# Kernel tuning notes

Measured on AMD Instinct MI355X. Metric: run time of the kernel, lower is better.

Reference implementation:

```python
import jax, jax.numpy as jnp
import numpy as np

# Module hyperparams (from init_kwargs)
MAX_DISP = 4
DILA = 1
P = 2 * MAX_DISP // DILA + 1  # patch_size = 9 -> 81 output channels


def setup_inputs() -> dict:
    key = jax.random.key(0)
    k0, k1 = jax.random.split(key)
    B, C, H, W = 4, 256, 96, 160
    return {
        "fmap0": jax.random.normal(k0, (B, C, H, W), dtype=jnp.float32),
        "fmap1": jax.random.normal(k1, (B, C, H, W), dtype=jnp.float32),
    }


def reference(fmap0, fmap1):
    """SpatialCorrelationSampler(kernel_size=1, patch_size=P, stride=1,
    padding=0, dilation=1, dilation_patch=DILA), reshaped to (B, P*P, H, W).

    corr[b, p, y, x] = sum_c fmap0[b,c,y,x] * fmap1[b,c,y+dy_p,x+dx_p]
    with (dy,dx) in {-MAX_DISP..MAX_DISP step DILA}; out-of-bounds -> 0
    (no channel normalization, matching the CUDA sampler).
    """
    B, C, H, W = fmap0.shape
    D = MAX_DISP
    # Zero-pad fmap1 so every displacement is a static-size slice.
    padded = jnp.pad(fmap1, ((0, 0), (0, 0), (D, D), (D, D)))
    oy, ox = jnp.meshgrid(jnp.arange(P) * DILA, jnp.arange(P) * DILA, indexing="ij")
    offs = jnp.stack([oy.ravel(), ox.ravel()], axis=1)  # (P*P, 2)

    def one_disp(off):
        # window of fmap1 shifted by (off - D): (B, C, H, W)
        win = jax.lax.dynamic_slice(padded, (0, 0, off[0], off[1]), (B, C, H, W))
        return jnp.einsum("bchw,bchw->bhw", fmap0, win)

    corr = jax.lax.map(one_disp, offs)  # (P*P, B, H, W), avoids P^2*C blowup
    return jnp.transpose(corr, (1, 0, 2, 3))  # (B, P*P, H, W)
```

## Files before the change

### kernel.cpp

```cpp
#include <hip/hip_runtime.h>


#define Bn 4
#define Cn 256
#define Hn 96
#define Wn 160
#define HWn (Hn * Wn)
#define NP 81
#define TY 16
#define TX 16
#define CCH 8
#define NSTAGE (Cn / CCH)
#define WROWS (TY + 8)
#define SEGS 6
#define LROW 28
#define F1C (WROWS * LROW)
#define BUF (CCH * F1C)
#define NT 576
#define F1STG (CCH * HWn / 4)

__global__ __launch_bounds__(NT, 2) void corr_kernel(const float* __restrict__ f0,
                                                     const float* __restrict__ f1,
                                                     float* __restrict__ out) {
    __shared__ __align__(16) float lds[2 * BUF];

    const int tid  = threadIdx.x;
    const int wave = tid >> 6;
    const int lane = tid & 63;
    const int r    = lane >> 2;
    const int g    = lane & 3;

    const int blk = blockIdx.x;
    const int xcd = blk & 7;
    const int it  = blk >> 3;
    const int b   = xcd >> 1;
    const int ty  = (xcd & 1) * 3 + it / 10;
    const int tx  = it % 10;
    const int y0  = ty * TY;
    const int x0  = tx * TX;

    const int scc  = tid / (WROWS * SEGS);
    const int srm  = tid - scc * (WROWS * SEGS);
    const int srr  = srm / SEGS;
    const int sseg = srm - srr * SEGS;
    const int sgy  = y0 - 4 + srr;
    const int sgx  = x0 - 4 + sseg * 4;
    const bool sval = (sgy >= 0) && (sgy < Hn) && (sgx >= 0) && (sgx < Wn);
    const int slidx = (scc * F1C + srr * LROW + sseg * 4) >> 2;
    const int sgidx = sval ? ((((b * Cn + scc) * Hn + sgy) * Wn + sgx) >> 2) : 0;

    const float4* __restrict__ f1v = (const float4*)f1;
    float4* lv = (float4*)lds;

    float4 p1a = make_float4(0.f, 0.f, 0.f, 0.f), p1b = p1a;
    if (sval) { p1a = f1v[sgidx]; p1b = f1v[sgidx + HWn]; }

    const float* f0s = f0 + ((b * Cn) * Hn + y0 + r) * Wn + x0 + g * 4;
    float4 p0[CCH];
#pragma unroll
    for (int cc = 0; cc < CCH; ++cc) p0[cc] = *(const float4*)(f0s + cc * HWn);

    float acc[9][4];
#pragma unroll
    for (int i = 0; i < 9; ++i)
#pragma unroll
        for (int j = 0; j < 4; ++j) acc[i][j] = 0.f;

    for (int s = 0; s < NSTAGE; ++s) {
        float4* buf = lv + (s & 1) * (BUF / 4);
        buf[slidx]       = p1a;
        buf[slidx + F1C] = p1b;
        __syncthreads();

        const int ns = (s + 1 < NSTAGE) ? s + 1 : NSTAGE - 1;
        float4 n1a = make_float4(0.f, 0.f, 0.f, 0.f), n1b = n1a;
        if (sval) { n1a = f1v[sgidx + ns * F1STG]; n1b = f1v[sgidx + ns * F1STG + HWn]; }
        float4 n0[CCH];
#pragma unroll
        for (int cc = 0; cc < CCH; ++cc)
            n0[cc] = *(const float4*)(f0s + (ns * CCH + cc) * HWn);

        const float* base = &lds[(s & 1) * BUF + (r + wave) * LROW + g * 4];
#pragma unroll
        for (int cc = 0; cc < CCH; ++cc) {
            const float* wr = base + cc * F1C;
            float4 w0 = *(const float4*)(wr);
            float4 w1 = *(const float4*)(wr + 4);
            float4 w2 = *(const float4*)(wr + 8);
            float av[4]  = {p0[cc].x, p0[cc].y, p0[cc].z, p0[cc].w};
            float wv[12] = {w0.x, w0.y, w0.z, w0.w, w1.x, w1.y, w1.z, w1.w,
                            w2.x, w2.y, w2.z, w2.w};
#pragma unroll
            for (int dx = 0; dx < 9; ++dx)
#pragma unroll
                for (int rx = 0; rx < 4; ++rx)
                    acc[dx][rx] = fmaf(av[rx], wv[rx + dx], acc[dx][rx]);
        }

        p1a = n1a; p1b = n1b;
#pragma unroll
        for (int cc = 0; cc < CCH; ++cc) p0[cc] = n0[cc];
    }

    const int orow = ((b * NP + wave * 9) * Hn + y0 + r) * Wn + x0 + g * 4;
#pragma unroll
    for (int dx = 0; dx < 9; ++dx)
        *(float4*)(out + orow + dx * HWn) =
            make_float4(acc[dx][0], acc[dx][1], acc[dx][2], acc[dx][3]);
}

extern "C" void kernel_launch(void* const* d_in, const int* in_sizes, int n_in,
                              void* d_out, int out_size, void* d_ws, size_t ws_size,
                              hipStream_t stream) {
    const float* f0 = (const float*)d_in[0];
    const float* f1 = (const float*)d_in[1];
    float* out = (float*)d_out;
    corr_kernel<<<dim3(240), NT, 0, stream>>>(f0, f1, out);
}
```

Baseline: 182.8 us.

## Rewrite correlation as fp16 MFMA banded matmul over channel chunks

Replaces the scalar FP32 FMA correlation kernel with one that converts both feature maps to fp16 and computes 16x32 banded products with 16x16x32 f16 MFMA instructions. Each wave handles one output row, and a 32-wide window is kept per displacement row, so only the diagonal band of each product is written out. Tiling, grid size (480 blocks of 512 threads) and the LDS layout all change. Much of the computed tile is thrown away, and the fp16 inputs reduce accuracy of a 256-channel sum.

```diff
diff --git a/kernel.cpp b/kernel.cpp
--- a/kernel.cpp
+++ b/kernel.cpp
@@ -1,5 +1,9 @@
 #include <hip/hip_runtime.h>
 
+
+using pkh2_t  = __attribute__((ext_vector_type(2))) __fp16;
+using half8_t = __attribute__((ext_vector_type(8))) _Float16;
+using f32x4_t = __attribute__((ext_vector_type(4))) float;
 
 #define Bn 4
 #define Cn 256
@@ -7,106 +11,120 @@
 #define Wn 160
 #define HWn (Hn * Wn)
 #define NP 81
-#define TY 16
-#define TX 16
-#define CCH 8
-#define NSTAGE (Cn / CCH)
-#define WROWS (TY + 8)
-#define SEGS 6
-#define LROW 28
-#define F1C (WROWS * LROW)
-#define BUF (CCH * F1C)
-#define NT 576
-#define F1STG (CCH * HWn / 4)
+#define YS 8
+#define MT 16
+#define KC 32
+#define NCHK (Cn / KC)
+#define WR (YS + 8)
+#define WP 32
+#define PXD 20
+#define ROWD (WP * PXD)
+#define BUFD (WR * ROWD)
+#define NT 512
 
-__global__ __launch_bounds__(NT, 2) void corr_kernel(const float* __restrict__ f0,
-                                                     const float* __restrict__ f1,
-                                                     float* __restrict__ out) {
-    __shared__ __align__(16) float lds[2 * BUF];
+__global__ __launch_bounds__(NT, 2) void corr_mfma(const float* __restrict__ f0,
+                                                   const float* __restrict__ f1,
+                                                   float* __restrict__ out) {
+    __shared__ __align__(16) unsigned int lds[BUFD];
 
     const int tid  = threadIdx.x;
-    const int wave = tid >> 6;
+    const int w    = tid >> 6;
     const int lane = tid & 63;
-    const int r    = lane >> 2;
-    const int g    = lane & 3;
+    const int q    = lane >> 4;
+    const int n    = lane & 15;
 
     const int blk = blockIdx.x;
     const int xcd = blk & 7;
     const int it  = blk >> 3;
     const int b   = xcd >> 1;
-    const int ty  = (xcd & 1) * 3 + it / 10;
-    const int tx  = it % 10;
-    const int y0  = ty * TY;
-    const int x0  = tx * TX;
+    const int ys  = (xcd & 1) * 6 + it / 10;
+    const int xt  = it % 10;
+    const int y0  = ys * YS;
+    const int x0  = xt * MT;
+    const int y   = y0 + w;
 
-    const int scc  = tid / (WROWS * SEGS);
-    const int srm  = tid - scc * (WROWS * SEGS);
-    const int srr  = srm / SEGS;
-    const int sseg = srm - srr * SEGS;
-    const int sgy  = y0 - 4 + srr;
-    const int sgx  = x0 - 4 + sseg * 4;
-    const bool sval = (sgy >= 0) && (sgy < Hn) && (sgx >= 0) && (sgx < Wn);
-    const int slidx = (scc * F1C + srr * LROW + sseg * 4) >> 2;
-    const int sgidx = sval ? ((((b * Cn + scc) * Hn + sgy) * Wn + sgx) >> 2) : 0;
+    const int rr  = tid >> 5;
+    const int pxg = (tid >> 2) & 7;
+    const int cs  = tid & 3;
+    const int gy  = y0 - 4 + rr;
+    const int gx  = x0 - 8 + pxg * 4;
+    const bool sv = (gy >= 0) && (gy < Hn) && (gx >= 0) && (gx < Wn);
+    const float4* __restrict__ f1v = (const float4*)f1;
+    const int sg0 = sv ? ((((b * Cn) * Hn + gy) * Wn + gx) >> 2) : 0;
+    const int ldw = rr * ROWD + (pxg * 4) * PXD + cs * 4;
 
-    const float4* __restrict__ f1v = (const float4*)f1;
-    float4* lv = (float4*)lds;
+    const float* __restrict__ f0p = f0 + (b * Cn) * HWn + y * Wn + x0 + n;
 
-    float4 p1a = make_float4(0.f, 0.f, 0.f, 0.f), p1b = p1a;
-    if (sval) { p1a = f1v[sgidx]; p1b = f1v[sgidx + HWn]; }
+    f32x4_t acc[9][2];
+#pragma unroll
+    for (int d = 0; d < 9; ++d)
+#pragma unroll
+        for (int t = 0; t < 2; ++t) acc[d][t] = (f32x4_t){0.f, 0.f, 0.f, 0.f};
 
-    const float* f0s = f0 + ((b * Cn) * Hn + y0 + r) * Wn + x0 + g * 4;
-    float4 p0[CCH];
+    float4 F[8];
+    float  A[8];
 #pragma unroll
-    for (int cc = 0; cc < CCH; ++cc) p0[cc] = *(const float4*)(f0s + cc * HWn);
+    for (int j = 0; j < 8; ++j) {
+        const int c = cs * 8 + j;
+        F[j] = sv ? f1v[sg0 + c * (HWn / 4)] : make_float4(0.f, 0.f, 0.f, 0.f);
+        A[j] = f0p[(q * 8 + j) * HWn];
+    }
 
-    float acc[9][4];
+    for (int ch = 0; ch < NCHK; ++ch) {
+        __syncthreads();
 #pragma unroll
-    for (int i = 0; i < 9; ++i)
+        for (int i = 0; i < 4; ++i) {
+            union { pkh2_t h2[4]; uint4 u4; } u;
 #pragma unroll
-        for (int j = 0; j < 4; ++j) acc[i][j] = 0.f;
-
-    for (int s = 0; s < NSTAGE; ++s) {
-        float4* buf = lv + (s & 1) * (BUF / 4);
-        buf[slidx]       = p1a;
-        buf[slidx + F1C] = p1b;
+            for (int k = 0; k < 4; ++k) {
+                const float lo = ((const float*)&F[2 * k])[i];
+                const float hi = ((const float*)&F[2 * k + 1])[i];
+                u.h2[k] = __builtin_amdgcn_cvt_pkrtz(lo, hi);
+            }
+            *(uint4*)&lds[ldw + i * PXD] = u.u4;
+        }
+        union { pkh2_t h2[4]; half8_t h8; } ua;
+#pragma unroll
+        for (int k = 0; k < 4; ++k)
+            ua.h2[k] = __builtin_amdgcn_cvt_pkrtz(A[2 * k], A[2 * k + 1]);
+        const half8_t afrag = ua.h8;
         __syncthreads();
 
-        const int ns = (s + 1 < NSTAGE) ? s + 1 : NSTAGE - 1;
-        float4 n1a = make_float4(0.f, 0.f, 0.f, 0.f), n1b = n1a;
-        if (sval) { n1a = f1v[sgidx + ns * F1STG]; n1b = f1v[sgidx + ns * F1STG + HWn]; }
-        float4 n0[CCH];
+        if (ch + 1 < NCHK) {
+            const int cb = (ch + 1) * KC;
 #pragma unroll
-        for (int cc = 0; cc < CCH; ++cc)
-            n0[cc] = *(const float4*)(f0s + (ns * CCH + cc) * HWn);
-
-        const float* base = &lds[(s & 1) * BUF + (r + wave) * LROW + g * 4];
-#pragma unroll
-        for (int cc = 0; cc < CCH; ++cc) {
-            const float* wr = base + cc * F1C;
-            float4 w0 = *(const float4*)(wr);
-            float4 w1 = *(const float4*)(wr + 4);
-            float4 w2 = *(const float4*)(wr + 8);
-            float av[4]  = {p0[cc].x, p0[cc].y, p0[cc].z, p0[cc].w};
-            float wv[12] = {w0.x, w0.y, w0.z, w0.w, w1.x, w1.y, w1.z, w1.w,
-                            w2.x, w2.y, w2.z, w2.w};
-#pragma unroll
-            for (int dx = 0; dx < 9; ++dx)
-#pragma unroll
-                for (int rx = 0; rx < 4; ++rx)
-                    acc[dx][rx] = fmaf(av[rx], wv[rx + dx], acc[dx][rx]);
+            for (int j = 0; j < 8; ++j) {
+                const int c = cb + cs * 8 + j;
+                F[j] = sv ? f1v[sg0 + c * (HWn / 4)] : make_float4(0.f, 0.f, 0.f, 0.f);
+                A[j] = f0p[(cb + q * 8 + j) * HWn];
+            }
         }
 
-        p1a = n1a; p1b = n1b;
 #pragma unroll
-        for (int cc = 0; cc < CCH; ++cc) p0[cc] = n0[cc];
+        for (int d = 0; d < 9; ++d) {
+            const unsigned int* rp = &lds[(w + d) * ROWD + n * PXD + q * 4];
+#pragma unroll
+            for (int t = 0; t < 2; ++t) {
+                const half8_t bfrag = *(const half8_t*)(rp + t * 16 * PXD);
+                acc[d][t] = __builtin_amdgcn_mfma_f32_16x16x32_f16(afrag, bfrag,
+                                                                   acc[d][t], 0, 0, 0);
+            }
+        }
     }
 
-    const int orow = ((b * NP + wave * 9) * Hn + y0 + r) * Wn + x0 + g * 4;
 #pragma unroll
-    for (int dx = 0; dx < 9; ++dx)
-        *(float4*)(out + orow + dx * HWn) =
-            make_float4(acc[dx][0], acc[dx][1], acc[dx][2], acc[dx][3]);
+    for (int d = 0; d < 9; ++d)
+#pragma unroll
+        for (int t = 0; t < 2; ++t)
+#pragma unroll
+            for (int r = 0; r < 4; ++r) {
+                const int m  = q * 4 + r;
+                const int dx = t * 16 + n - 8 - m;
+                if (dx >= -4 && dx <= 4) {
+                    const int p = d * 9 + dx + 4;
+                    out[((b * NP + p) * Hn + y) * Wn + x0 + m] = acc[d][t][r];
+                }
+            }
 }
 
 extern "C" void kernel_launch(void* const* d_in, const int* in_sizes, int n_in,
@@ -115,5 +133,5 @@
     const float* f0 = (const float*)d_in[0];
     const float* f1 = (const float*)d_in[1];
     float* out = (float*)d_out;
-    corr_kernel<<<dim3(240), NT, 0, stream>>>(f0, f1, out);
+    corr_mfma<<<dim3(480), NT, 0, stream>>>(f0, f1, out);
 }
```

Result: slower. 187.9 us (+2.8%).
